# Performance work log

Measured on AMD Instinct MI355X. Metric: run time of the kernel, lower is better.

The kernel has to match this reference:

```python
import jax, jax.numpy as jnp
import numpy as np


def setup_inputs() -> dict:
    key = jax.random.key(0)
    k1, k2 = jax.random.split(key)
    B, F, Ci, R = 16, 1024, 64, 1
    Co, K = 64, 4
    ll = jax.random.normal(k1, (B, F, Ci, R), dtype=jnp.float32)
    logits = jax.random.normal(k2, (Co, Ci, K, K, R), dtype=jnp.float32)
    return {"ll": ll, "logits": logits}


def reference(ll, logits):
    # ll: (B, F, Ci, R)   logits: (Co, Ci, K, K, R)
    B, F, Ci, R = ll.shape
    Co, _, K, _, _ = logits.shape
    H = W = int(F ** 0.5)
    OH, OW = H // K, W // K
    # normalize weights over input channels (sum_dim=1)
    lw = jax.nn.log_softmax(logits, axis=1)  # (Co, Ci, K, K, R)
    # b (h w) ci r -> b ci h w r
    x = ll.reshape(B, H, W, Ci, R).transpose(0, 3, 1, 2, 4)
    # b ci (oh kh) (ow kw) r -> b ci oh ow kh kw r
    x = x.reshape(B, Ci, OH, K, OW, K, R).transpose(0, 1, 2, 4, 3, 5, 6)
    # broadcast-add log-weights (shared over oh, ow) then logsumexp over ci
    weighted = x[:, None] + lw[None, :, :, None, None, :, :, :]  # (B, Co, Ci, OH, OW, K, K, R)
    res = jax.scipy.special.logsumexp(weighted, axis=2)          # (B, Co, OH, OW, K, K, R)
    # b co oh ow kh kw r -> b (oh kh ow kw) co r
    out = res.transpose(0, 2, 4, 3, 5, 1, 6).reshape(B, F, Co, R)
    return out
```

## Files before the change

kernel.cpp:

```cpp
#include <hip/hip_runtime.h>

#define CI 64
#define CO 64
#define F_ 1024
#define KK 4
#define NPAT 16

__global__ __launch_bounds__(256) void prep_kernel(
    const float* __restrict__ logits, float* __restrict__ E, float* __restrict__ Lsum)
{
    __shared__ float part[4 * CO];
    const int pat = blockIdx.x;
    const int t   = threadIdx.x;
    const int co  = t & 63;
    const int q   = t >> 6;
    const float* lg = logits + co * (CI * KK * KK) + pat;
    float psum = 0.f;
    #pragma unroll
    for (int i = 0; i < 16; ++i) {
        const int ci = q * 16 + i;
        const float e = __expf(lg[ci * (KK * KK)]);
        E[pat * (CI * CO) + ci * CO + co] = e;
        psum += e;
    }
    part[q * CO + co] = psum;
    __syncthreads();
    if (q == 0) {
        const float tot = (part[co] + part[CO + co]) + (part[2 * CO + co] + part[3 * CO + co]);
        Lsum[pat * CO + co] = __logf(tot);
    }
}

__global__ __launch_bounds__(256, 4) void main_kernel(
    const float* __restrict__ ll, const float* __restrict__ E,
    const float* __restrict__ Lsum, float* __restrict__ out)
{
    __shared__ float p_lds[4][4][CI];
    const int tid   = threadIdx.x;
    const int lane  = tid & 63;
    const int wv    = tid >> 6;
    const int bid   = blockIdx.x;
    const int pat   = bid & (NPAT - 1);
    const int chunk = bid >> 4;
    const int kh = pat >> 2, kw = pat & 3;

    int   idx[4];
    float p[4];
    #pragma unroll
    for (int j = 0; j < 4; ++j) {
        const int pr = (chunk << 4) + (wv << 2) + j;
        const int b  = pr >> 6;
        const int oh = (pr >> 3) & 7;
        const int ow = pr & 7;
        const int f  = (oh * 4 + kh) * 32 + (ow * 4 + kw);
        idx[j] = (b * F_ + f) * CI + lane;
        p[j]   = ll[idx[j]];
    }

    const float* Ep = E + pat * (CI * CO) + lane;
    float wreg[CI];
    #pragma unroll
    for (int ci = 0; ci < CI; ++ci) wreg[ci] = Ep[ci * CO];
    const float lsum = Lsum[pat * CO + lane];

    #pragma unroll
    for (int j = 0; j < 4; ++j) {
        p[j] = __expf(p[j]);
        p_lds[wv][j][lane] = p[j];
    }
    __builtin_amdgcn_wave_barrier();

    float a0[4] = {0.f, 0.f, 0.f, 0.f}, a1[4] = {0.f, 0.f, 0.f, 0.f};
    #pragma unroll
    for (int ci = 0; ci < CI; ci += 4) {
        #pragma unroll
        for (int j = 0; j < 4; ++j) {
            const float4 pv = *reinterpret_cast<const float4*>(&p_lds[wv][j][ci]);
            a0[j] = fmaf(pv.x, wreg[ci + 0], a0[j]);
            a1[j] = fmaf(pv.y, wreg[ci + 1], a1[j]);
            a0[j] = fmaf(pv.z, wreg[ci + 2], a0[j]);
            a1[j] = fmaf(pv.w, wreg[ci + 3], a1[j]);
        }
    }
    #pragma unroll
    for (int j = 0; j < 4; ++j)
        out[idx[j]] = __logf(a0[j] + a1[j]) - lsum;
}

extern "C" void kernel_launch(void* const* d_in, const int* in_sizes, int n_in,
                              void* d_out, int out_size, void* d_ws, size_t ws_size,
                              hipStream_t stream) {
    const float* ll     = (const float*)d_in[0];
    const float* logits = (const float*)d_in[1];
    float* out  = (float*)d_out;
    float* E    = (float*)d_ws;
    float* Lsum = E + NPAT * CI * CO;
    prep_kernel<<<dim3(NPAT), dim3(256), 0, stream>>>(logits, E, Lsum);
    main_kernel<<<dim3(1024), dim3(256), 0, stream>>>(ll, E, Lsum, out);
}
```

Baseline: 64.97 us.

## Replace LDS staging with readlane broadcast, vectorize weight loads, compute log-sum inline

The main kernel no longer stages exp(ll) through shared memory. Each channel value is broadcast across the wave with readlane, which becomes scalar operands to the FMAs. The prep kernel now writes E interleaved in groups of four input channels, so each lane loads its weights as sixteen float4 reads. The normalizer log-sum is recomputed per thread from those registers instead of being read from a separate buffer, and the prep kernel is spread over 64 blocks. This removes LDS traffic and the extra reduction, but the readlanes are serialized scalar operations and register pressure rises with four accumulators per output.

After: 64.06 us. Within noise of the previous version (-1.4%).

```diff
diff --git a/kernel.cpp b/kernel.cpp
--- a/kernel.cpp
+++ b/kernel.cpp
@@ -6,36 +6,30 @@
 #define KK 4
 #define NPAT 16
 
+__device__ __forceinline__ float bcast(float v, int l) {
+    return __int_as_float(__builtin_amdgcn_readlane(__float_as_int(v), l));
+}
+
 __global__ __launch_bounds__(256) void prep_kernel(
-    const float* __restrict__ logits, float* __restrict__ E, float* __restrict__ Lsum)
+    const float* __restrict__ logits, float* __restrict__ E)
 {
-    __shared__ float part[4 * CO];
-    const int pat = blockIdx.x;
+    const int pat = blockIdx.x >> 2;
+    const int q   = blockIdx.x & 3;
     const int t   = threadIdx.x;
     const int co  = t & 63;
-    const int q   = t >> 6;
-    const float* lg = logits + co * (CI * KK * KK) + pat;
-    float psum = 0.f;
+    const int i   = t >> 6;
     #pragma unroll
-    for (int i = 0; i < 16; ++i) {
-        const int ci = q * 16 + i;
-        const float e = __expf(lg[ci * (KK * KK)]);
-        E[pat * (CI * CO) + ci * CO + co] = e;
-        psum += e;
-    }
-    part[q * CO + co] = psum;
-    __syncthreads();
-    if (q == 0) {
-        const float tot = (part[co] + part[CO + co]) + (part[2 * CO + co] + part[3 * CO + co]);
-        Lsum[pat * CO + co] = __logf(tot);
+    for (int k = 0; k < 4; ++k) {
+        const int ci = q * 16 + i * 4 + k;
+        const float e = __expf(logits[co * (CI * KK * KK) + ci * (KK * KK) + pat]);
+        E[pat * (CI * CO) + (ci >> 2) * (CO * 4) + co * 4 + (ci & 3)] = e;
     }
 }
 
 __global__ __launch_bounds__(256, 4) void main_kernel(
     const float* __restrict__ ll, const float* __restrict__ E,
-    const float* __restrict__ Lsum, float* __restrict__ out)
+    float* __restrict__ out)
 {
-    __shared__ float p_lds[4][4][CI];
     const int tid   = threadIdx.x;
     const int lane  = tid & 63;
     const int wv    = tid >> 6;
@@ -57,34 +51,43 @@
         p[j]   = ll[idx[j]];
     }
 
-    const float* Ep = E + pat * (CI * CO) + lane;
+    float4 wv4[16];
+    const float4* Ep4 = reinterpret_cast<const float4*>(E + pat * (CI * CO)) + lane;
+    #pragma unroll
+    for (int g = 0; g < 16; ++g) wv4[g] = Ep4[g * CO];
     float wreg[CI];
     #pragma unroll
-    for (int ci = 0; ci < CI; ++ci) wreg[ci] = Ep[ci * CO];
-    const float lsum = Lsum[pat * CO + lane];
+    for (int g = 0; g < 16; ++g) {
+        wreg[4 * g + 0] = wv4[g].x; wreg[4 * g + 1] = wv4[g].y;
+        wreg[4 * g + 2] = wv4[g].z; wreg[4 * g + 3] = wv4[g].w;
+    }
+
+    float ts[8];
+    #pragma unroll
+    for (int i = 0; i < 8; ++i)
+        ts[i] = (wreg[i] + wreg[i + 8]) + (wreg[i + 16] + wreg[i + 24])
+              + (wreg[i + 32] + wreg[i + 40]) + (wreg[i + 48] + wreg[i + 56]);
+    const float lsum = __logf(((ts[0] + ts[1]) + (ts[2] + ts[3]))
+                            + ((ts[4] + ts[5]) + (ts[6] + ts[7])));
 
     #pragma unroll
-    for (int j = 0; j < 4; ++j) {
-        p[j] = __expf(p[j]);
-        p_lds[wv][j][lane] = p[j];
-    }
-    __builtin_amdgcn_wave_barrier();
+    for (int j = 0; j < 4; ++j) p[j] = __expf(p[j]);
 
-    float a0[4] = {0.f, 0.f, 0.f, 0.f}, a1[4] = {0.f, 0.f, 0.f, 0.f};
+    float a0[4] = {0.f,0.f,0.f,0.f}, a1[4] = {0.f,0.f,0.f,0.f};
+    float a2[4] = {0.f,0.f,0.f,0.f}, a3[4] = {0.f,0.f,0.f,0.f};
     #pragma unroll
     for (int ci = 0; ci < CI; ci += 4) {
         #pragma unroll
         for (int j = 0; j < 4; ++j) {
-            const float4 pv = *reinterpret_cast<const float4*>(&p_lds[wv][j][ci]);
-            a0[j] = fmaf(pv.x, wreg[ci + 0], a0[j]);
-            a1[j] = fmaf(pv.y, wreg[ci + 1], a1[j]);
-            a0[j] = fmaf(pv.z, wreg[ci + 2], a0[j]);
-            a1[j] = fmaf(pv.w, wreg[ci + 3], a1[j]);
+            a0[j] = fmaf(bcast(p[j], ci + 0), wreg[ci + 0], a0[j]);
+            a1[j] = fmaf(bcast(p[j], ci + 1), wreg[ci + 1], a1[j]);
+            a2[j] = fmaf(bcast(p[j], ci + 2), wreg[ci + 2], a2[j]);
+            a3[j] = fmaf(bcast(p[j], ci + 3), wreg[ci + 3], a3[j]);
         }
     }
     #pragma unroll
     for (int j = 0; j < 4; ++j)
-        out[idx[j]] = __logf(a0[j] + a1[j]) - lsum;
+        out[idx[j]] = __logf((a0[j] + a1[j]) + (a2[j] + a3[j])) - lsum;
 }
 
 extern "C" void kernel_launch(void* const* d_in, const int* in_sizes, int n_in,
@@ -92,9 +95,8 @@
                               hipStream_t stream) {
     const float* ll     = (const float*)d_in[0];
     const float* logits = (const float*)d_in[1];
-    float* out  = (float*)d_out;
-    float* E    = (float*)d_ws;
-    float* Lsum = E + NPAT * CI * CO;
-    prep_kernel<<<dim3(NPAT), dim3(256), 0, stream>>>(logits, E, Lsum);
-    main_kernel<<<dim3(1024), dim3(256), 0, stream>>>(ll, E, Lsum, out);
+    float* out = (float*)d_out;
+    float* E   = (float*)d_ws;
+    prep_kernel<<<dim3(64), dim3(256), 0, stream>>>(logits, E);
+    main_kernel<<<dim3(1024), dim3(256), 0, stream>>>(ll, E, out);
 }
```
